# Optimization experiments

Hardware: AMD Instinct MI355X
Metric: run time of the kernel (lower is better)

The kernel has to match this reference:

```python
import jax, jax.numpy as jnp
import numpy as np

EPS = 0.05        # entropic regularization
TEMP = 0.1        # softmax temperature
ITERS = 3         # min sinkhorn iterations
TOL = 1e-3        # convergence tolerance
MAX_ITERS = 100   # max sinkhorn iterations
TINY = 1e-12

B, K, C = 4096, 3000, 8


def _sinkhorn(scores):
    """Balanced assignments Q[B,K]: rows sum ~1, cols sum ~B/K. Detached."""
    Bn, Kn = scores.shape
    S = scores.astype(jnp.float32) / EPS
    S = S - jnp.max(S, axis=1, keepdims=True)
    Q = jnp.exp(S)
    target_c = jnp.float32(Bn / Kn)

    def cond(state):
        _, _, _, done = state
        return jnp.logical_not(done)

    def body(state):
        u, v, it, _ = state
        u = 1.0 / (Q @ v.T + TINY)              # [B,1], a = ones
        v = target_c / (u.T @ Q + TINY)          # [1,K], b = B/K * ones
        it = it + 1
        P = u * Q * v
        row_err = jnp.max(jnp.abs(jnp.sum(P, axis=1) - 1.0))
        col_err = jnp.max(jnp.abs(jnp.sum(P, axis=0) - target_c))
        err = jnp.maximum(row_err, col_err)
        done = (it >= ITERS) & ((it >= MAX_ITERS) | (err <= TOL))
        return (u, v, it, done)

    u0 = jnp.ones((Bn, 1), jnp.float32)
    v0 = jnp.ones((1, Kn), jnp.float32)
    u, v, _, _ = jax.lax.while_loop(cond, body, (u0, v0, jnp.int32(0), jnp.bool_(False)))
    P = u * Q * v
    P = P / jnp.clip(jnp.sum(P, axis=1, keepdims=True), TINY, None)
    P = P * (target_c / jnp.clip(jnp.sum(P, axis=0, keepdims=True), TINY, None))
    P = P / jnp.clip(jnp.sum(P, axis=1, keepdims=True), TINY, None)
    return jax.lax.stop_gradient(P)


def setup_inputs() -> dict:
    key = jax.random.key(0)
    keys = jax.random.split(key, C)
    inp = {f"logits{c}": jax.random.normal(keys[c], (B, K), dtype=jnp.float32)
           for c in range(C)}
    inp["idx_a"] = 0
    inp["idx_b"] = 1
    return inp


def reference(logits0, logits1, logits2, logits3, logits4, logits5, logits6, logits7, idx_a, idx_b):
    crops = [logits0, logits1, logits2, logits3, logits4, logits5, logits6, logits7]
    Qa = _sinkhorn(crops[idx_a])
    Qb = _sinkhorn(crops[idx_b])

    def entropy(Q):
        return -jnp.mean(jnp.sum(Q * jnp.log(Q + TINY), axis=1))

    ent = 0.5 * (entropy(Qa) + entropy(Qb))
    q_max_mean = 0.5 * (jnp.mean(jnp.max(Qa, axis=1)) + jnp.mean(jnp.max(Qb, axis=1)))

    losses = []
    for c, lg in enumerate(crops):
        logp = jax.nn.log_softmax(lg.astype(jnp.float32) / TEMP, axis=1)
        if c != idx_a:
            losses.append(-jnp.mean(jnp.sum(Qa * logp, axis=1)))
        if c != idx_b:
            losses.append(-jnp.mean(jnp.sum(Qb * logp, axis=1)))
    loss = jnp.mean(jnp.stack(losses))
    return (loss, ent, q_max_mean)
```

## Files before the change

### kernel.cpp

```cpp
#include <hip/hip_runtime.h>
#include <hip/hip_cooperative_groups.h>
#include <math.h>

namespace cg = cooperative_groups;

struct Ptr8 { const float* p[8]; };

#define Bn 4096
#define Kn 3000
#define KQ4 750
#define KP 3072
#define INV_EPS 20.0f
#define INV_TEMP 10.0f
#define TINYF 1e-12f
#define TOLF 1e-3f
#define TGTC (4096.0f/3000.0f)

#define CAPR 448
#define CAPC 448
#define CUTF 1.4f

#define BLD_NBLK 2048

#define IT_NBLK 64
#define IT_THR 1024
#define IT_NWAVE (IT_NBLK * IT_THR / 64)
#define MAXC 6
#define MAXR 8

#define NSTR 12
#define NCH 40
#define GRID_S 480
#define NW_S (GRID_S * 4)

__device__ __forceinline__ float wsum(float x) {
#pragma unroll
  for (int o = 32; o; o >>= 1) x += __shfl_xor(x, o, 64);
  return x;
}
__device__ __forceinline__ float wmax(float x) {
#pragma unroll
  for (int o = 32; o; o >>= 1) x = fmaxf(x, __shfl_xor(x, o, 64));
  return x;
}
__device__ __forceinline__ float block_max(float x) {
  __shared__ float s[4];
  x = wmax(x);
  if ((threadIdx.x & 63) == 0) s[threadIdx.x >> 6] = x;
  __syncthreads();
  float r = fmaxf(fmaxf(s[0], s[1]), fmaxf(s[2], s[3]));
  __syncthreads();
  return r;
}

__device__ __forceinline__ float2 block_max2_16(float x0, float x1, float2* sh) {
  x0 = wmax(x0); x1 = wmax(x1);
  if ((threadIdx.x & 63) == 0) sh[threadIdx.x >> 6] = make_float2(x0, x1);
  __syncthreads();
  float m0 = sh[0].x, m1 = sh[0].y;
#pragma unroll
  for (int i = 1; i < 16; ++i) { m0 = fmaxf(m0, sh[i].x); m1 = fmaxf(m1, sh[i].y); }
  __syncthreads();
  return make_float2(m0, m1);
}

__device__ __forceinline__ void gbar(unsigned* bar, unsigned& genl) {
  __syncthreads();
  if (threadIdx.x == 0) {
    unsigned g = ++genl;
    __threadfence();
    unsigned arr = __hip_atomic_fetch_add(&bar[0], 1u, __ATOMIC_ACQ_REL, __HIP_MEMORY_SCOPE_AGENT);
    if (arr == IT_NBLK - 1) {
      __hip_atomic_store(&bar[0], 0u, __ATOMIC_RELAXED, __HIP_MEMORY_SCOPE_AGENT);
      __hip_atomic_store(&bar[1], g, __ATOMIC_RELEASE, __HIP_MEMORY_SCOPE_AGENT);
    } else {
      while ((int)(__hip_atomic_load(&bar[1], __ATOMIC_ACQUIRE, __HIP_MEMORY_SCOPE_AGENT) - g) < 0)
        __builtin_amdgcn_s_sleep(1);
    }
    __threadfence();
  }
  __syncthreads();
}

struct BuildArgs {
  Ptr8 ptrs;
  const int* iap; const int* ibp;
  float* pmA; float* pmB;
  float* r; float* rinv;
  unsigned* rowcnt;
  unsigned* colcnt;
  float* csrq; unsigned short* csridx;
  float* cscq; unsigned short* cscidx;
};

__global__ __launch_bounds__(256, 2) void build_sparse(BuildArgs a) {
  const int tid = threadIdx.x;
  const int lane = tid & 63;
  const int wv = blockIdx.x * 4 + (tid >> 6);
  const int crop = wv >> 12;
  const int row = wv & (Bn - 1);
  const int idx = ((crop ? *a.ibp : *a.iap) & 7);
  const float* __restrict__ lg = a.ptrs.p[idx];
  const float4* rp = (const float4*)(lg + (size_t)row * Kn);

  float M = -INFINITY, T = 0.f;
  for (int i = lane; i < KQ4; i += 64) {
    float4 x = rp[i];
    float m4 = fmaxf(fmaxf(x.x, x.y), fmaxf(x.z, x.w));
    float t4 = __expf((x.x - m4) * INV_EPS) + __expf((x.y - m4) * INV_EPS)
             + __expf((x.z - m4) * INV_EPS) + __expf((x.w - m4) * INV_EPS);
    float Mn = fmaxf(M, m4);
    T = T * __expf((M - Mn) * INV_EPS) + t4 * __expf((m4 - Mn) * INV_EPS);
    M = Mn;
  }
#pragma unroll
  for (int o = 32; o; o >>= 1) {
    float M2 = __shfl_xor(M, o, 64);
    float T2 = __shfl_xor(T, o, 64);
    float Mn = fmaxf(M, M2);
    T = T * __expf((M - Mn) * INV_EPS) + T2 * __expf((M2 - Mn) * INV_EPS);
    M = Mn;
  }
  if (lane == 0) {
    (crop ? a.pmB : a.pmA)[row] = M;
    a.r[crop * Bn + row] = T;
    a.rinv[crop * Bn + row] = 1.0f / (T + TINYF);
  }
  const float thr = M - CUTF;

  int cnt = 0;
  for (int i = lane; i < KQ4; i += 64) {
    float4 x = rp[i];
    cnt += (x.x >= thr) + (x.y >= thr) + (x.z >= thr) + (x.w >= thr);
  }
  int incl = cnt;
#pragma unroll
  for (int o = 1; o < 64; o <<= 1) {
    int t = __shfl_up(incl, o, 64);
    if (lane >= o) incl += t;
  }
  int total = __shfl(incl, 63, 64);
  int p = incl - cnt;
  if (lane == 0) a.rowcnt[crop * Bn + row] = (unsigned)min(total, CAPR);

  float* crow = a.csrq + ((size_t)crop * Bn + row) * CAPR;
  unsigned short* cidx = a.csridx + ((size_t)crop * Bn + row) * CAPR;
  unsigned* ccnt = a.colcnt + crop * KP;
  float* cq_ = a.cscq + (size_t)crop * KP * CAPC;
  unsigned short* ci_ = a.cscidx + (size_t)crop * KP * CAPC;

  for (int i = lane; i < KQ4; i += 64) {
    float4 x = rp[i];
    int k0 = i * 4;
#define EMIT(val, kk)                                                          \
    if ((val) >= thr) {                                                        \
      float q = __expf(((val) - M) * INV_EPS);                                 \
      if (p < CAPR) { crow[p] = q; cidx[p] = (unsigned short)(kk); }           \
      unsigned slot = atomicAdd(&ccnt[kk], 1u);                                \
      if (slot < CAPC) {                                                       \
        size_t o2 = (size_t)(kk) * CAPC + slot;                                \
        cq_[o2] = q; ci_[o2] = (unsigned short)row;                            \
      }                                                                        \
      ++p;                                                                     \
    }
    EMIT(x.x, k0 + 0) EMIT(x.y, k0 + 1) EMIT(x.z, k0 + 2) EMIT(x.w, k0 + 3)
#undef EMIT
  }
}

struct ItArgs {
  float* pAa; float* pCa; float* pAb; float* pCb;
  float* u; float* r; float* rinv; float* v; float* alpha;
  const unsigned* rowcnt; const unsigned* colcnt;
  const float* csrq; const unsigned short* csridx;
  const float* cscq; const unsigned short* cscidx;
  unsigned* errA; unsigned* errB;
  unsigned* bar;
};

__global__ __launch_bounds__(IT_THR) void sinkhorn_iterate(ItArgs a) {
  const int tid = threadIdx.x;
  const int lane = tid & 63;
  const int wv = blockIdx.x * (IT_THR / 64) + (tid >> 6);

  __shared__ float2 sred[16];
  __shared__ float serr[4];

  int cN[MAXC], cCrop[MAXC];
#pragma unroll
  for (int s = 0; s < MAXC; ++s) {
    int vc = wv + s * IT_NWAVE;
    if (vc < 2 * Kn) {
      int crop = vc >= Kn;
      cCrop[s] = crop;
      cN[s] = min((int)a.colcnt[crop * KP + (vc - crop * Kn)], CAPC);
    } else { cCrop[s] = -1; cN[s] = 0; }
  }
  int rN[MAXR];
#pragma unroll
  for (int s = 0; s < MAXR; ++s) {
    int vr = wv + s * IT_NWAVE;
    rN[s] = min((int)a.rowcnt[vr], CAPR);
  }

  unsigned genl = 0;
  bool done0 = false, done1 = false;
  int it = 0;
  while (true) {
    ++it;
    float cerr0 = 0.f, cerr1 = 0.f;
#pragma unroll
    for (int s = 0; s < MAXC; ++s) {
      int cc = cCrop[s];
      if (cc < 0) continue;
      if (cc ? done1 : done0) continue;
      int vc = wv + s * IT_NWAVE;
      int col = vc - cc * Kn;
      size_t base = ((size_t)cc * KP + col) * CAPC;
      const float* q = a.cscq + base;
      const unsigned short* ix = a.cscidx + base;
      const float* rb = a.rinv + cc * Bn;
      int n = cN[s];
      float acc = 0.f;
      for (int j = lane; j < n; j += 64) acc += q[j] * rb[ix[j]];
      acc = wsum(acc);
      float vk = TGTC / (acc + TINYF);
      if (lane == 0) a.v[cc * KP + col] = vk;
      float e = fabsf(vk * acc - TGTC);
      if (cc) cerr1 = fmaxf(cerr1, e); else cerr0 = fmaxf(cerr0, e);
    }
    if (it >= 3) {
      float2 bm = block_max2_16(cerr0, cerr1, sred);
      if (tid == 0) {
        if (!done0) atomicMax(&a.errA[2 * it + 1], __float_as_uint(bm.x));
        if (!done1) atomicMax(&a.errB[2 * it + 1], __float_as_uint(bm.y));
      }
    }
    gbar(a.bar, genl);
    float lerr0 = 0.f, lerr1 = 0.f;
#pragma unroll
    for (int s = 0; s < MAXR; ++s) {
      int vr = wv + s * IT_NWAVE;
      int crop = vr >= Bn;
      if (crop ? done1 : done0) continue;
      size_t base = (size_t)vr * CAPR;
      const float* q = a.csrq + base;
      const unsigned short* ix = a.csridx + base;
      const float* vb = a.v + crop * KP;
      int n = rN[s];
      float acc = 0.f;
      for (int j = lane; j < n; j += 64) acc += q[j] * vb[ix[j]];
      acc = wsum(acc);
      float uu = a.rinv[vr];
      if (lane == 0) {
        a.u[vr] = uu; a.r[vr] = acc;
        a.rinv[vr] = 1.0f / (acc + TINYF);
      }
      float e = fabsf(uu * acc - 1.0f);
      if (crop) lerr1 = fmaxf(lerr1, e); else lerr0 = fmaxf(lerr0, e);
    }
    if (it >= 3) {
      float2 bm = block_max2_16(lerr0, lerr1, sred);
      if (tid == 0) {
        if (!done0) atomicMax(&a.errA[2 * it], __float_as_uint(bm.x));
        if (!done1) atomicMax(&a.errB[2 * it], __float_as_uint(bm.y));
      }
    }
    gbar(a.bar, genl);
    if (it >= 3) {
      if (tid == 0) {
        serr[0] = __uint_as_float(__hip_atomic_load(&a.errA[2 * it], __ATOMIC_RELAXED, __HIP_MEMORY_SCOPE_AGENT));
        serr[1] = __uint_as_float(__hip_atomic_load(&a.errA[2 * it + 1], __ATOMIC_RELAXED, __HIP_MEMORY_SCOPE_AGENT));
        serr[2] = __uint_as_float(__hip_atomic_load(&a.errB[2 * it], __ATOMIC_RELAXED, __HIP_MEMORY_SCOPE_AGENT));
        serr[3] = __uint_as_float(__hip_atomic_load(&a.errB[2 * it + 1], __ATOMIC_RELAXED, __HIP_MEMORY_SCOPE_AGENT));
      }
      __syncthreads();
      if (!done0) done0 = (it >= 100) || (fmaxf(serr[0], serr[1]) <= TOLF);
      if (!done1) done1 = (it >= 100) || (fmaxf(serr[2], serr[3]) <= TOLF);
      __syncthreads();
      if (done0 && done1) break;
    }
  }

  for (int g = blockIdx.x * IT_THR + tid; g < 2 * Bn; g += IT_NBLK * IT_THR) {
    float uu = a.u[g], rr = a.r[g];
    a.alpha[g] = uu / fmaxf(uu * rr, TINYF);
  }
  gbar(a.bar, genl);
#pragma unroll
  for (int s = 0; s < MAXC; ++s) {
    int cc = cCrop[s];
    if (cc < 0) continue;
    int vc = wv + s * IT_NWAVE;
    int col = vc - cc * Kn;
    size_t base = ((size_t)cc * KP + col) * CAPC;
    const float* q = a.cscq + base;
    const unsigned short* ix = a.cscidx + base;
    const float* al = a.alpha + cc * Bn;
    int n = cN[s];
    float d = 0.f;
    for (int j = lane; j < n; j += 64) d += q[j] * al[ix[j]];
    d = wsum(d);
    float vk = a.v[cc * KP + col];
    if (lane == 0)
      (cc ? a.pCb : a.pCa)[col] = vk * TGTC / fmaxf(vk * d, TINYF);
  }
  gbar(a.bar, genl);
#pragma unroll
  for (int s = 0; s < MAXR; ++s) {
    int vr = wv + s * IT_NWAVE;
    int crop = vr >= Bn;
    size_t base = (size_t)vr * CAPR;
    const float* q = a.csrq + base;
    const unsigned short* ix = a.csridx + base;
    const float* pc = crop ? a.pCb : a.pCa;
    int n = rN[s];
    float e = 0.f;
    for (int j = lane; j < n; j += 64) e += q[j] * pc[ix[j]];
    e = wsum(e);
    if (lane == 0) {
      float al = a.alpha[vr];
      (crop ? a.pAb : a.pAa)[vr - crop * Bn] = al / fmaxf(al * e, TINYF);
    }
  }
}

__global__ __launch_bounds__(256, 2) void sinkhorn_dense(
    Ptr8 ptrs, const int* __restrict__ idxp,
    float* __restrict__ ws_m, float* __restrict__ ws_u, float* __restrict__ ws_r,
    float* __restrict__ ws_A, float* __restrict__ ws_v, float* __restrict__ ws_C,
    float* __restrict__ cpart, unsigned* __restrict__ errbuf)
{
  cg::grid_group grid = cg::this_grid();
  const int idx = (*idxp) & 7;
  const float* __restrict__ lg = ptrs.p[idx];
  const int tid = threadIdx.x;
  const int lane = tid & 63;
  const int gw = blockIdx.x * 4 + (tid >> 6);
  const int stripe = blockIdx.x % NSTR;
  const int chunk = blockIdx.x / NSTR;
  const int kcol = stripe * 256 + tid;
  const int rs = (chunk * Bn) / NCH;
  const int re = ((chunk + 1) * Bn) / NCH;

  for (int row = gw; row < Bn; row += NW_S) {
    const float4* rp = (const float4*)(lg + (size_t)row * Kn);
    float M = -INFINITY, T = 0.f;
    for (int i = lane; i < KQ4; i += 64) {
      float4 x = rp[i];
      float m4 = fmaxf(fmaxf(x.x, x.y), fmaxf(x.z, x.w));
      float t4 = __expf((x.x - m4) * INV_EPS) + __expf((x.y - m4) * INV_EPS)
               + __expf((x.z - m4) * INV_EPS) + __expf((x.w - m4) * INV_EPS);
      float Mn = fmaxf(M, m4);
      T = T * __expf((M - Mn) * INV_EPS) + t4 * __expf((m4 - Mn) * INV_EPS);
      M = Mn;
    }
#pragma unroll
    for (int o = 32; o; o >>= 1) {
      float M2 = __shfl_xor(M, o, 64);
      float T2 = __shfl_xor(T, o, 64);
      float Mn = fmaxf(M, M2);
      T = T * __expf((M - Mn) * INV_EPS) + T2 * __expf((M2 - Mn) * INV_EPS);
      M = Mn;
    }
    if (lane == 0) { ws_m[row] = M; ws_r[row] = T; }
  }
  grid.sync(); __threadfence();

  int it = 0;
  while (true) {
    ++it;
    {
      float acc = 0.f;
      if (kcol < Kn) {
        for (int row = rs; row < re; ++row) {
          float u = 1.0f / (ws_r[row] + TINYF);
          acc += u * __expf((lg[(size_t)row * Kn + kcol] - ws_m[row]) * INV_EPS);
        }
      }
      cpart[chunk * KP + stripe * 256 + tid] = acc;
    }
    grid.sync(); __threadfence();
    {
      int k = blockIdx.x * 256 + tid;
      float cerr = 0.f;
      if (k < Kn) {
        float c = 0.f;
        for (int ch = 0; ch < NCH; ++ch) c += cpart[ch * KP + k];
        float vk = TGTC / (c + TINYF);
        ws_v[k] = vk;
        cerr = fabsf(vk * c - TGTC);
      }
      float bm = block_max(cerr);
      if (tid == 0) atomicMax(&errbuf[2 * it + 1], __float_as_uint(bm));
    }
    grid.sync(); __threadfence();
    {
      float lerr = 0.f;
      for (int row = gw; row < Bn; row += NW_S) {
        const float4* rp = (const float4*)(lg + (size_t)row * Kn);
        const float4* vp = (const float4*)ws_v;
        float mm = ws_m[row];
        float u = 1.0f / (ws_r[row] + TINYF);
        float Ssum = 0.f;
        for (int i = lane; i < KQ4; i += 64) {
          float4 x = rp[i];
          float4 vv = vp[i];
          Ssum += __expf((x.x - mm) * INV_EPS) * vv.x
                + __expf((x.y - mm) * INV_EPS) * vv.y
                + __expf((x.z - mm) * INV_EPS) * vv.z
                + __expf((x.w - mm) * INV_EPS) * vv.w;
        }
        Ssum = wsum(Ssum);
        if (lane == 0) { ws_u[row] = u; ws_r[row] = Ssum; }
        lerr = fmaxf(lerr, fabsf(u * Ssum - 1.0f));
      }
      float bm = block_max(lerr);
      if (tid == 0) atomicMax(&errbuf[2 * it], __float_as_uint(bm));
    }
    grid.sync(); __threadfence();
    unsigned rbits = __hip_atomic_load(&errbuf[2 * it], __ATOMIC_RELAXED, __HIP_MEMORY_SCOPE_AGENT);
    unsigned cbits = __hip_atomic_load(&errbuf[2 * it + 1], __ATOMIC_RELAXED, __HIP_MEMORY_SCOPE_AGENT);
    float err = fmaxf(__uint_as_float(rbits), __uint_as_float(cbits));
    if (it >= 3 && (it >= 100 || err <= TOLF)) break;
  }

  {
    float acc = 0.f;
    if (kcol < Kn) {
      for (int row = rs; row < re; ++row) {
        float u = ws_u[row];
        float sp = fmaxf(u * ws_r[row], TINYF);
        acc += (u / sp) * __expf((lg[(size_t)row * Kn + kcol] - ws_m[row]) * INV_EPS);
      }
    }
    cpart[chunk * KP + stripe * 256 + tid] = acc;
  }
  grid.sync(); __threadfence();
  {
    int k = blockIdx.x * 256 + tid;
    if (k < Kn) {
      float d = 0.f;
      for (int ch = 0; ch < NCH; ++ch) d += cpart[ch * KP + k];
      float vk = ws_v[k];
      ws_C[k] = vk * TGTC / fmaxf(vk * d, TINYF);
    }
  }
  grid.sync(); __threadfence();
  {
    for (int row = gw; row < Bn; row += NW_S) {
      const float4* rp = (const float4*)(lg + (size_t)row * Kn);
      const float4* cp = (const float4*)ws_C;
      float mm = ws_m[row];
      float e = 0.f;
      for (int i = lane; i < KQ4; i += 64) {
        float4 x = rp[i];
        float4 cc = cp[i];
        e += __expf((x.x - mm) * INV_EPS) * cc.x
           + __expf((x.y - mm) * INV_EPS) * cc.y
           + __expf((x.z - mm) * INV_EPS) * cc.z
           + __expf((x.w - mm) * INV_EPS) * cc.w;
      }
      e = wsum(e);
      if (lane == 0) {
        float u = ws_u[row];
        float sp = fmaxf(u * ws_r[row], TINYF);
        float us = u / sp;
        float w = us * e;
        ws_A[row] = us / fmaxf(w, TINYF);
      }
    }
  }
}

__global__ __launch_bounds__(256) void loss_kernel(
    Ptr8 ptrs, const int* __restrict__ iap, const int* __restrict__ ibp,
    const float* __restrict__ wsa, const float* __restrict__ wsb,
    float* __restrict__ out)
{
  const int ia = (*iap) & 7;
  const int ib = (*ibp) & 7;
  const int lane = threadIdx.x & 63;
  const int row = blockIdx.x * 4 + (threadIdx.x >> 6);

  const float ma = wsa[row];
  const float Aa = wsa[4096 + row];
  const float mb = wsb[row];
  const float Ab = wsb[4096 + row];
  const float4* Ca4 = (const float4*)(wsa + 8192);
  const float4* Cb4 = (const float4*)(wsb + 8192);
  size_t off = (size_t)row * Kn;
  const float4* X4[8];
#pragma unroll
  for (int c = 0; c < 8; ++c) X4[c] = (const float4*)(ptrs.p[c] + off);
  const float4* xa4 = (const float4*)(ptrs.p[ia] + off);
  const float4* xb4 = (const float4*)(ptrs.p[ib] + off);

  float M[8], S[8], da[8], db[8];
#pragma unroll
  for (int c = 0; c < 8; ++c) { M[c] = -INFINITY; S[c] = 0.f; da[c] = 0.f; db[c] = 0.f; }
  float enta = 0.f, entb = 0.f, ra = 0.f, rb = 0.f, qam = 0.f, qbm = 0.f;

  for (int i = lane; i < KQ4; i += 64) {
    float4 xa = xa4[i], xb = xb4[i];
    float4 ca = Ca4[i], cb = Cb4[i];
    float qa0 = __expf((xa.x - ma) * INV_EPS) * Aa * ca.x;
    float qa1 = __expf((xa.y - ma) * INV_EPS) * Aa * ca.y;
    float qa2 = __expf((xa.z - ma) * INV_EPS) * Aa * ca.z;
    float qa3 = __expf((xa.w - ma) * INV_EPS) * Aa * ca.w;
    float qb0 = __expf((xb.x - mb) * INV_EPS) * Ab * cb.x;
    float qb1 = __expf((xb.y - mb) * INV_EPS) * Ab * cb.y;
    float qb2 = __expf((xb.z - mb) * INV_EPS) * Ab * cb.z;
    float qb3 = __expf((xb.w - mb) * INV_EPS) * Ab * cb.w;
    ra += (qa0 + qa1) + (qa2 + qa3);
    rb += (qb0 + qb1) + (qb2 + qb3);
    enta += qa0 * __logf(qa0 + TINYF) + qa1 * __logf(qa1 + TINYF)
          + qa2 * __logf(qa2 + TINYF) + qa3 * __logf(qa3 + TINYF);
    entb += qb0 * __logf(qb0 + TINYF) + qb1 * __logf(qb1 + TINYF)
          + qb2 * __logf(qb2 + TINYF) + qb3 * __logf(qb3 + TINYF);
    qam = fmaxf(qam, fmaxf(fmaxf(qa0, qa1), fmaxf(qa2, qa3)));
    qbm = fmaxf(qbm, fmaxf(fmaxf(qb0, qb1), fmaxf(qb2, qb3)));
#pragma unroll
    for (int c = 0; c < 8; ++c) {
      float4 x = X4[c][i];
      float y0 = x.x * INV_TEMP, y1 = x.y * INV_TEMP;
      float y2 = x.z * INV_TEMP, y3 = x.w * INV_TEMP;
      float m4 = fmaxf(fmaxf(y0, y1), fmaxf(y2, y3));
      float t4 = __expf(y0 - m4) + __expf(y1 - m4) + __expf(y2 - m4) + __expf(y3 - m4);
      float Mn = fmaxf(M[c], m4);
      S[c] = S[c] * __expf(M[c] - Mn) + t4 * __expf(m4 - Mn);
      M[c] = Mn;
      da[c] += qa0 * x.x + qa1 * x.y + qa2 * x.z + qa3 * x.w;
      db[c] += qb0 * x.x + qb1 * x.y + qb2 * x.z + qb3 * x.w;
    }
  }

#pragma unroll
  for (int c = 0; c < 8; ++c) {
#pragma unroll
    for (int o = 32; o; o >>= 1) {
      float M2 = __shfl_xor(M[c], o, 64);
      float S2 = __shfl_xor(S[c], o, 64);
      float Mn = fmaxf(M[c], M2);
      S[c] = S[c] * __expf(M[c] - Mn) + S2 * __expf(M2 - Mn);
      M[c] = Mn;
    }
    da[c] = wsum(da[c]);
    db[c] = wsum(db[c]);
  }
  enta = wsum(enta); entb = wsum(entb);
  ra = wsum(ra); rb = wsum(rb);
  qam = wmax(qam); qbm = wmax(qbm);

  if (lane == 0) {
    float lsum = 0.f;
    int nt = 0;
#pragma unroll
    for (int c = 0; c < 8; ++c) {
      float L = M[c] + __logf(S[c]);
      if (c != ia) { lsum -= INV_TEMP * da[c] - L * ra; ++nt; }
      if (c != ib) { lsum -= INV_TEMP * db[c] - L * rb; ++nt; }
    }
    atomicAdd(&out[0], lsum / ((float)nt * (float)Bn));
    atomicAdd(&out[1], -0.5f / (float)Bn * (enta + entb));
    atomicAdd(&out[2], 0.5f / (float)Bn * (qam + qbm));
  }
}

extern "C" void kernel_launch(void* const* d_in, const int* in_sizes, int n_in,
                              void* d_out, int out_size, void* d_ws, size_t ws_size,
                              hipStream_t stream)
{
  (void)in_sizes; (void)n_in; (void)out_size;
  Ptr8 ptrs;
  for (int c = 0; c < 8; ++c) ptrs.p[c] = (const float*)d_in[c];
  const int* iap = (const int*)d_in[8];
  const int* ibp = (const int*)d_in[9];
  float* ws = (float*)d_ws;
  float* out = (float*)d_out;

  float* PA = ws;
  float* PB = ws + 11264;
  float* u_ = ws + 22528;
  float* r_ = ws + 30720;
  float* ri_ = ws + 38912;
  float* v_ = ws + 47104;
  float* al = ws + 53248;
  unsigned* rowcnt = (unsigned*)(ws + 61440);
  unsigned* colcnt = (unsigned*)(ws + 69632);
  unsigned* errA = (unsigned*)(ws + 75776);
  unsigned* errB = (unsigned*)(ws + 76288);
  unsigned* bar = (unsigned*)(ws + 76800);
  float* csrq = ws + 76864;
  unsigned short* csridx = (unsigned short*)(ws + 3746880);
  float* cscq = ws + 5581888;
  unsigned short* cscidx = (unsigned short*)(ws + 8334400);
  const size_t need_bytes = (size_t)9710656 * 4;

  hipMemsetAsync(colcnt, 0, 7232 * sizeof(unsigned), stream);
  hipMemsetAsync(d_out, 0, 3 * sizeof(float), stream);

  if (ws_size >= need_bytes) {
    BuildArgs ba;
    ba.ptrs = ptrs; ba.iap = iap; ba.ibp = ibp;
    ba.pmA = PA; ba.pmB = PB;
    ba.r = r_; ba.rinv = ri_;
    ba.rowcnt = rowcnt; ba.colcnt = colcnt;
    ba.csrq = csrq; ba.csridx = csridx; ba.cscq = cscq; ba.cscidx = cscidx;
    hipLaunchKernelGGL(build_sparse, dim3(BLD_NBLK), dim3(256), 0, stream, ba);

    ItArgs ia;
    ia.pAa = PA + 4096; ia.pCa = PA + 8192;
    ia.pAb = PB + 4096; ia.pCb = PB + 8192;
    ia.u = u_; ia.r = r_; ia.rinv = ri_; ia.v = v_; ia.alpha = al;
    ia.rowcnt = rowcnt; ia.colcnt = colcnt;
    ia.csrq = csrq; ia.csridx = csridx; ia.cscq = cscq; ia.cscidx = cscidx;
    ia.errA = errA; ia.errB = errB; ia.bar = bar;
    void* args1[] = { (void*)&ia };
    hipLaunchCooperativeKernel((const void*)sinkhorn_iterate, dim3(IT_NBLK), dim3(IT_THR),
                               (void**)args1, 0u, stream);
  } else {
    float* cpart = ws + 76864;
    {
      float* m = PA; float* A = PA + 4096; float* C = PA + 8192;
      void* args[] = { (void*)&ptrs, (void*)&iap, (void*)&m, (void*)&u_, (void*)&r_,
                       (void*)&A, (void*)&v_, (void*)&C, (void*)&cpart, (void*)&errA };
      hipLaunchCooperativeKernel((const void*)sinkhorn_dense, dim3(GRID_S), dim3(256),
                                 (void**)args, 0u, stream);
    }
    {
      float* m = PB; float* A = PB + 4096; float* C = PB + 8192;
      void* args[] = { (void*)&ptrs, (void*)&ibp, (void*)&m, (void*)&u_, (void*)&r_,
                       (void*)&A, (void*)&v_, (void*)&C, (void*)&cpart, (void*)&errB };
      hipLaunchCooperativeKernel((const void*)sinkhorn_dense, dim3(GRID_S), dim3(256),
                                 (void**)args, 0u, stream);
    }
  }

  loss_kernel<<<dim3(Bn / 4), dim3(256), 0, stream>>>(ptrs, iap, ibp, PA, PB, out);
}
```

Baseline: 4.726 ms.

## Cache scaling vectors in LDS and replace atomic grid barrier with flag-based barrier

The iterate kernel now copies the full rinv and v vectors into shared memory each half-iteration, so the sparse gathers read LDS instead of scattered global memory. The atomic-counter grid barrier is replaced by per-block arrive flags polled by block 0 plus a release word. Per-block error maxima are stored in slots and reduced by every block, replacing the global atomicMax. Each block now recomputes reciprocals for all rows every iteration and uses a large LDS footprint, which adds redundant work and depends on relaxed-atomic visibility being correct.

Measured after the change: 3.788 ms. -19.8%, faster.

```diff
diff --git a/kernel.cpp b/kernel.cpp
--- a/kernel.cpp
+++ b/kernel.cpp
@@ -27,6 +27,10 @@
 #define IT_NWAVE (IT_NBLK * IT_THR / 64)
 #define MAXC 6
 #define MAXR 8
+#define BARSTRIDE 32
+
+#define ALD(p)    __hip_atomic_load((p), __ATOMIC_RELAXED, __HIP_MEMORY_SCOPE_AGENT)
+#define AST(p, x) __hip_atomic_store((p), (x), __ATOMIC_RELAXED, __HIP_MEMORY_SCOPE_AGENT)
 
 #define NSTR 12
 #define NCH 40
@@ -53,40 +57,11 @@
   return r;
 }
 
-__device__ __forceinline__ float2 block_max2_16(float x0, float x1, float2* sh) {
-  x0 = wmax(x0); x1 = wmax(x1);
-  if ((threadIdx.x & 63) == 0) sh[threadIdx.x >> 6] = make_float2(x0, x1);
-  __syncthreads();
-  float m0 = sh[0].x, m1 = sh[0].y;
-#pragma unroll
-  for (int i = 1; i < 16; ++i) { m0 = fmaxf(m0, sh[i].x); m1 = fmaxf(m1, sh[i].y); }
-  __syncthreads();
-  return make_float2(m0, m1);
-}
-
-__device__ __forceinline__ void gbar(unsigned* bar, unsigned& genl) {
-  __syncthreads();
-  if (threadIdx.x == 0) {
-    unsigned g = ++genl;
-    __threadfence();
-    unsigned arr = __hip_atomic_fetch_add(&bar[0], 1u, __ATOMIC_ACQ_REL, __HIP_MEMORY_SCOPE_AGENT);
-    if (arr == IT_NBLK - 1) {
-      __hip_atomic_store(&bar[0], 0u, __ATOMIC_RELAXED, __HIP_MEMORY_SCOPE_AGENT);
-      __hip_atomic_store(&bar[1], g, __ATOMIC_RELEASE, __HIP_MEMORY_SCOPE_AGENT);
-    } else {
-      while ((int)(__hip_atomic_load(&bar[1], __ATOMIC_ACQUIRE, __HIP_MEMORY_SCOPE_AGENT) - g) < 0)
-        __builtin_amdgcn_s_sleep(1);
-    }
-    __threadfence();
-  }
-  __syncthreads();
-}
-
 struct BuildArgs {
   Ptr8 ptrs;
   const int* iap; const int* ibp;
   float* pmA; float* pmB;
-  float* r; float* rinv;
+  float* r;
   unsigned* rowcnt;
   unsigned* colcnt;
   float* csrq; unsigned short* csridx;
@@ -124,7 +99,6 @@
   if (lane == 0) {
     (crop ? a.pmB : a.pmA)[row] = M;
     a.r[crop * Bn + row] = T;
-    a.rinv[crop * Bn + row] = 1.0f / (T + TINYF);
   }
   const float thr = M - CUTF;
 
@@ -170,21 +144,45 @@
 
 struct ItArgs {
   float* pAa; float* pCa; float* pAb; float* pCb;
-  float* u; float* r; float* rinv; float* v; float* alpha;
+  float* u; float* r; float* v;
   const unsigned* rowcnt; const unsigned* colcnt;
   const float* csrq; const unsigned short* csridx;
   const float* cscq; const unsigned short* cscidx;
-  unsigned* errA; unsigned* errB;
-  unsigned* bar;
+  unsigned* err;
+  unsigned* arrive;
+  unsigned* release;
 };
+
+__device__ __forceinline__ void gbar2(unsigned* arrive, unsigned* release, unsigned g) {
+  __syncthreads();
+  if (threadIdx.x == 0)
+    AST(&arrive[blockIdx.x * BARSTRIDE], g);
+  if (blockIdx.x == 0) {
+    if (threadIdx.x < 64) {
+      while ((int)(ALD(&arrive[threadIdx.x * BARSTRIDE]) - g) < 0)
+        __builtin_amdgcn_s_sleep(1);
+    }
+    __syncthreads();
+    if (threadIdx.x == 0) AST(release, g);
+  } else {
+    if (threadIdx.x == 0) {
+      while ((int)(ALD(release) - g) < 0)
+        __builtin_amdgcn_s_sleep(1);
+    }
+  }
+  __syncthreads();
+}
 
 __global__ __launch_bounds__(IT_THR) void sinkhorn_iterate(ItArgs a) {
   const int tid = threadIdx.x;
   const int lane = tid & 63;
-  const int wv = blockIdx.x * (IT_THR / 64) + (tid >> 6);
-
+  const int bid = blockIdx.x;
+  const int wv = bid * (IT_THR / 64) + (tid >> 6);
+
+  __shared__ float lds_rinv[2 * Bn];
+  __shared__ float lds_v[2 * KP];
   __shared__ float2 sred[16];
-  __shared__ float serr[4];
+  __shared__ float serr[2];
 
   int cN[MAXC], cCrop[MAXC];
 #pragma unroll
@@ -203,11 +201,18 @@
     rN[s] = min((int)a.rowcnt[vr], CAPR);
   }
 
-  unsigned genl = 0;
+  unsigned gen = 0;
   bool done0 = false, done1 = false;
   int it = 0;
   while (true) {
     ++it;
+    const int par = it & 1;
+    for (int g = tid; g < 2 * Bn; g += IT_THR) {
+      int cr = g >> 12;
+      if (!(cr ? done1 : done0))
+        lds_rinv[g] = 1.0f / (ALD(&a.r[g]) + TINYF);
+    }
+    __syncthreads();
     float cerr0 = 0.f, cerr1 = 0.f;
 #pragma unroll
     for (int s = 0; s < MAXC; ++s) {
@@ -219,24 +224,34 @@
       size_t base = ((size_t)cc * KP + col) * CAPC;
       const float* q = a.cscq + base;
       const unsigned short* ix = a.cscidx + base;
-      const float* rb = a.rinv + cc * Bn;
       int n = cN[s];
       float acc = 0.f;
-      for (int j = lane; j < n; j += 64) acc += q[j] * rb[ix[j]];
+      for (int j = lane; j < n; j += 64) acc += q[j] * lds_rinv[cc * Bn + ix[j]];
       acc = wsum(acc);
       float vk = TGTC / (acc + TINYF);
-      if (lane == 0) a.v[cc * KP + col] = vk;
+      if (lane == 0) AST(&a.v[cc * KP + col], vk);
       float e = fabsf(vk * acc - TGTC);
       if (cc) cerr1 = fmaxf(cerr1, e); else cerr0 = fmaxf(cerr0, e);
     }
     if (it >= 3) {
-      float2 bm = block_max2_16(cerr0, cerr1, sred);
+      cerr0 = wmax(cerr0); cerr1 = wmax(cerr1);
+      if (lane == 0) sred[tid >> 6] = make_float2(cerr0, cerr1);
+      __syncthreads();
       if (tid == 0) {
-        if (!done0) atomicMax(&a.errA[2 * it + 1], __float_as_uint(bm.x));
-        if (!done1) atomicMax(&a.errB[2 * it + 1], __float_as_uint(bm.y));
-      }
-    }
-    gbar(a.bar, genl);
+        float m0 = sred[0].x, m1 = sred[0].y;
+#pragma unroll
+        for (int i = 1; i < 16; ++i) { m0 = fmaxf(m0, sred[i].x); m1 = fmaxf(m1, sred[i].y); }
+        if (!done0) AST(&a.err[par * 256 + 64 + bid], __float_as_uint(m0));
+        if (!done1) AST(&a.err[par * 256 + 192 + bid], __float_as_uint(m1));
+      }
+    }
+    gbar2(a.arrive, a.release, ++gen);
+    for (int g = tid; g < 2 * KP; g += IT_THR) {
+      int cr = g >= KP;
+      if (!(cr ? done1 : done0))
+        lds_v[g] = ALD(&a.v[g]);
+    }
+    __syncthreads();
     float lerr0 = 0.f, lerr1 = 0.f;
 #pragma unroll
     for (int s = 0; s < MAXR; ++s) {
@@ -246,47 +261,55 @@
       size_t base = (size_t)vr * CAPR;
       const float* q = a.csrq + base;
       const unsigned short* ix = a.csridx + base;
-      const float* vb = a.v + crop * KP;
       int n = rN[s];
       float acc = 0.f;
-      for (int j = lane; j < n; j += 64) acc += q[j] * vb[ix[j]];
+      for (int j = lane; j < n; j += 64) acc += q[j] * lds_v[crop * KP + ix[j]];
       acc = wsum(acc);
-      float uu = a.rinv[vr];
+      float uu = lds_rinv[vr];
       if (lane == 0) {
-        a.u[vr] = uu; a.r[vr] = acc;
-        a.rinv[vr] = 1.0f / (acc + TINYF);
+        AST(&a.u[vr], uu);
+        AST(&a.r[vr], acc);
       }
       float e = fabsf(uu * acc - 1.0f);
       if (crop) lerr1 = fmaxf(lerr1, e); else lerr0 = fmaxf(lerr0, e);
     }
     if (it >= 3) {
-      float2 bm = block_max2_16(lerr0, lerr1, sred);
+      lerr0 = wmax(lerr0); lerr1 = wmax(lerr1);
+      if (lane == 0) sred[tid >> 6] = make_float2(lerr0, lerr1);
+      __syncthreads();
       if (tid == 0) {
-        if (!done0) atomicMax(&a.errA[2 * it], __float_as_uint(bm.x));
-        if (!done1) atomicMax(&a.errB[2 * it], __float_as_uint(bm.y));
-      }
-    }
-    gbar(a.bar, genl);
+        float m0 = sred[0].x, m1 = sred[0].y;
+#pragma unroll
+        for (int i = 1; i < 16; ++i) { m0 = fmaxf(m0, sred[i].x); m1 = fmaxf(m1, sred[i].y); }
+        if (!done0) AST(&a.err[par * 256 + bid], __float_as_uint(m0));
+        if (!done1) AST(&a.err[par * 256 + 128 + bid], __float_as_uint(m1));
+      }
+    }
+    gbar2(a.arrive, a.release, ++gen);
     if (it >= 3) {
-      if (tid == 0) {
-        serr[0] = __uint_as_float(__hip_atomic_load(&a.errA[2 * it], __ATOMIC_RELAXED, __HIP_MEMORY_SCOPE_AGENT));
-        serr[1] = __uint_as_float(__hip_atomic_load(&a.errA[2 * it + 1], __ATOMIC_RELAXED, __HIP_MEMORY_SCOPE_AGENT));
-        serr[2] = __uint_as_float(__hip_atomic_load(&a.errB[2 * it], __ATOMIC_RELAXED, __HIP_MEMORY_SCOPE_AGENT));
-        serr[3] = __uint_as_float(__hip_atomic_load(&a.errB[2 * it + 1], __ATOMIC_RELAXED, __HIP_MEMORY_SCOPE_AGENT));
+      if (tid < 64) {
+        float e0 = __uint_as_float(ALD(&a.err[par * 256 + tid]));
+        float e1 = __uint_as_float(ALD(&a.err[par * 256 + 64 + tid]));
+        float e2 = __uint_as_float(ALD(&a.err[par * 256 + 128 + tid]));
+        float e3 = __uint_as_float(ALD(&a.err[par * 256 + 192 + tid]));
+        float eA = wmax(fmaxf(e0, e1));
+        float eB = wmax(fmaxf(e2, e3));
+        if (tid == 0) { serr[0] = eA; serr[1] = eB; }
       }
       __syncthreads();
-      if (!done0) done0 = (it >= 100) || (fmaxf(serr[0], serr[1]) <= TOLF);
-      if (!done1) done1 = (it >= 100) || (fmaxf(serr[2], serr[3]) <= TOLF);
+      if (!done0) done0 = (it >= 100) || (serr[0] <= TOLF);
+      if (!done1) done1 = (it >= 100) || (serr[1] <= TOLF);
       __syncthreads();
       if (done0 && done1) break;
     }
   }
 
-  for (int g = blockIdx.x * IT_THR + tid; g < 2 * Bn; g += IT_NBLK * IT_THR) {
-    float uu = a.u[g], rr = a.r[g];
-    a.alpha[g] = uu / fmaxf(uu * rr, TINYF);
-  }
-  gbar(a.bar, genl);
+  for (int g = tid; g < 2 * Bn; g += IT_THR) {
+    float uu = ALD(&a.u[g]);
+    float rr = ALD(&a.r[g]);
+    lds_rinv[g] = uu / fmaxf(uu * rr, TINYF);
+  }
+  __syncthreads();
 #pragma unroll
   for (int s = 0; s < MAXC; ++s) {
     int cc = cCrop[s];
@@ -296,16 +319,20 @@
     size_t base = ((size_t)cc * KP + col) * CAPC;
     const float* q = a.cscq + base;
     const unsigned short* ix = a.cscidx + base;
-    const float* al = a.alpha + cc * Bn;
     int n = cN[s];
     float d = 0.f;
-    for (int j = lane; j < n; j += 64) d += q[j] * al[ix[j]];
+    for (int j = lane; j < n; j += 64) d += q[j] * lds_rinv[cc * Bn + ix[j]];
     d = wsum(d);
-    float vk = a.v[cc * KP + col];
+    float vk = lds_v[cc * KP + col];
     if (lane == 0)
-      (cc ? a.pCb : a.pCa)[col] = vk * TGTC / fmaxf(vk * d, TINYF);
-  }
-  gbar(a.bar, genl);
+      AST(&(cc ? a.pCb : a.pCa)[col], vk * TGTC / fmaxf(vk * d, TINYF));
+  }
+  gbar2(a.arrive, a.release, ++gen);
+  for (int g = tid; g < 2 * KP; g += IT_THR) {
+    int cr = g >= KP;
+    lds_v[g] = ALD(&(cr ? a.pCb : a.pCa)[g - cr * KP]);
+  }
+  __syncthreads();
 #pragma unroll
   for (int s = 0; s < MAXR; ++s) {
     int vr = wv + s * IT_NWAVE;
@@ -313,13 +340,12 @@
     size_t base = (size_t)vr * CAPR;
     const float* q = a.csrq + base;
     const unsigned short* ix = a.csridx + base;
-    const float* pc = crop ? a.pCb : a.pCa;
     int n = rN[s];
     float e = 0.f;
-    for (int j = lane; j < n; j += 64) e += q[j] * pc[ix[j]];
+    for (int j = lane; j < n; j += 64) e += q[j] * lds_v[crop * KP + ix[j]];
     e = wsum(e);
     if (lane == 0) {
-      float al = a.alpha[vr];
+      float al = lds_rinv[vr];
       (crop ? a.pAb : a.pAa)[vr - crop * Bn] = al / fmaxf(al * e, TINYF);
     }
   }
@@ -583,28 +609,26 @@
   float* PB = ws + 11264;
   float* u_ = ws + 22528;
   float* r_ = ws + 30720;
-  float* ri_ = ws + 38912;
-  float* v_ = ws + 47104;
-  float* al = ws + 53248;
-  unsigned* rowcnt = (unsigned*)(ws + 61440);
-  unsigned* colcnt = (unsigned*)(ws + 69632);
-  unsigned* errA = (unsigned*)(ws + 75776);
-  unsigned* errB = (unsigned*)(ws + 76288);
-  unsigned* bar = (unsigned*)(ws + 76800);
-  float* csrq = ws + 76864;
-  unsigned short* csridx = (unsigned short*)(ws + 3746880);
-  float* cscq = ws + 5581888;
-  unsigned short* cscidx = (unsigned short*)(ws + 8334400);
-  const size_t need_bytes = (size_t)9710656 * 4;
-
-  hipMemsetAsync(colcnt, 0, 7232 * sizeof(unsigned), stream);
+  float* v_ = ws + 38912;
+  unsigned* rowcnt = (unsigned*)(ws + 45056);
+  unsigned* colcnt = (unsigned*)(ws + 53248);
+  unsigned* err = (unsigned*)(ws + 59392);
+  unsigned* arrive = (unsigned*)(ws + 59904);
+  unsigned* release = (unsigned*)(ws + 61952);
+  float* csrq = ws + 62016;
+  unsigned short* csridx = (unsigned short*)(ws + 3732032);
+  float* cscq = ws + 5567040;
+  unsigned short* cscidx = (unsigned short*)(ws + 8319552);
+  const size_t need_bytes = (size_t)9695808 * 4;
+
+  hipMemsetAsync(colcnt, 0, 8768 * sizeof(unsigned), stream);
   hipMemsetAsync(d_out, 0, 3 * sizeof(float), stream);
 
   if (ws_size >= need_bytes) {
     BuildArgs ba;
     ba.ptrs = ptrs; ba.iap = iap; ba.ibp = ibp;
     ba.pmA = PA; ba.pmB = PB;
-    ba.r = r_; ba.rinv = ri_;
+    ba.r = r_;
     ba.rowcnt = rowcnt; ba.colcnt = colcnt;
     ba.csrq = csrq; ba.csridx = csridx; ba.cscq = cscq; ba.cscidx = cscidx;
     hipLaunchKernelGGL(build_sparse, dim3(BLD_NBLK), dim3(256), 0, stream, ba);
@@ -612,15 +636,17 @@
     ItArgs ia;
     ia.pAa = PA + 4096; ia.pCa = PA + 8192;
     ia.pAb = PB + 4096; ia.pCb = PB + 8192;
-    ia.u = u_; ia.r = r_; ia.rinv = ri_; ia.v = v_; ia.alpha = al;
+    ia.u = u_; ia.r = r_; ia.v = v_;
     ia.rowcnt = rowcnt; ia.colcnt = colcnt;
     ia.csrq = csrq; ia.csridx = csridx; ia.cscq = cscq; ia.cscidx = cscidx;
-    ia.errA = errA; ia.errB = errB; ia.bar = bar;
+    ia.err = err; ia.arrive = arrive; ia.release = release;
     void* args1[] = { (void*)&ia };
     hipLaunchCooperativeKernel((const void*)sinkhorn_iterate, dim3(IT_NBLK), dim3(IT_THR),
                                (void**)args1, 0u, stream);
   } else {
-    float* cpart = ws + 76864;
+    float* cpart = ws + 62016;
+    unsigned* errA = err;
+    unsigned* errB = err + 256;
     {
       float* m = PA; float* A = PA + 4096; float* C = PA + 8192;
       void* args[] = { (void*)&ptrs, (void*)&iap, (void*)&m, (void*)&u_, (void*)&r_,
```
